# Kernel tuning notes

Measured on AMD Instinct MI355X. Metric: run time of the kernel, lower is better.

Reference implementation:

```python
import jax, jax.numpy as jnp
import numpy as np

HEADS = 12
DIM = 768


def setup_inputs() -> dict:
    key = jax.random.key(0)
    ks = jax.random.split(key, 11)
    B, T, D, H = 2, 2048, DIM, HEADS
    s = 0.02
    inp = {
        "x": jax.random.normal(ks[0], (B, T, D), dtype=jnp.float32),
        "Wq": jax.random.normal(ks[1], (D, D), dtype=jnp.float32) * s,
        "bq": jax.random.normal(ks[2], (D,), dtype=jnp.float32) * s,
        "Wk": jax.random.normal(ks[3], (D, D), dtype=jnp.float32) * s,
        "bk": jax.random.normal(ks[4], (D,), dtype=jnp.float32) * s,
        "Wv": jax.random.normal(ks[5], (D, D), dtype=jnp.float32) * s,
        "bv": jax.random.normal(ks[6], (D,), dtype=jnp.float32) * s,
        # shaped-attention affine params (torch init: alpha=1, beta=0, gamma=0;
        # perturb so all terms are exercised)
        "alpha": jnp.ones((1, H, 1, 1), jnp.float32) + 0.1 * jax.random.normal(ks[7], (1, H, 1, 1)),
        "beta": 0.1 * jax.random.normal(ks[8], (1, H, 1, 1), dtype=jnp.float32),
        "gamma": 0.1 * jax.random.normal(ks[9], (1, H, 1, 1), dtype=jnp.float32),
        # registered buffer C (zeros in the source)
        "C": jnp.zeros((H, 1, 1), jnp.float32),
    }
    return inp


def reference(x, Wq, bq, Wk, bk, Wv, bv, alpha, beta, gamma, C):
    B, T, D = x.shape
    H = HEADS
    hd = D // H
    scale = hd ** -0.5
    # torch nn.Linear: y = x @ W.T + b ; then [B,T,H,hd] -> [B,H,T,hd]
    q = (x @ Wq.T + bq).reshape(B, T, H, hd).transpose(0, 2, 1, 3)
    k = (x @ Wk.T + bk).reshape(B, T, H, hd).transpose(0, 2, 1, 3)
    v = (x @ Wv.T + bv).reshape(B, T, H, hd).transpose(0, 2, 1, 3)
    attn = jax.nn.softmax(jnp.einsum("bhqd,bhkd->bhqk", q, k) * scale, axis=-1)
    # shaped correction: alpha*I + beta*softmax - gamma*C
    eye = jnp.eye(T, dtype=x.dtype)
    attn = alpha * eye + beta * attn - gamma * C  # C:(H,1,1) broadcasts over T,T
    out = jnp.einsum("bhqk,bhkd->bhqd", attn, v)
    return out.transpose(0, 2, 1, 3).reshape(B, T, D)
```

## Files before the change

kernel.cpp:

```cpp
#include <hip/hip_runtime.h>
#include <hip/hip_bf16.h>

#define HEADS 12
#define HD 64
#define DMODEL 768
#define TSEQ 2048
#define BATCH 2
#define NTOK (BATCH*TSEQ)
#define NQKV (3*DMODEL)
#define KSPLIT 4
#define BK 64
#define KVBLK 64

typedef __attribute__((ext_vector_type(8))) short bf16x8;
typedef __attribute__((ext_vector_type(4))) short bf16x4;
typedef __attribute__((ext_vector_type(4))) float f32x4;
typedef __attribute__((ext_vector_type(16))) float f32x16;
typedef __attribute__((ext_vector_type(2))) unsigned uint32x2;

static __device__ inline float bf2f(short s) {
  union { float f; unsigned u; } cv; cv.u = ((unsigned)(unsigned short)s) << 16; return cv.f;
}
static __device__ inline short f2bf(float f) {
  union { float f; unsigned u; } cv; cv.f = f;
  unsigned u = cv.u;
  unsigned r = u + 0x7FFF + ((u >> 16) & 1);
  return (short)(r >> 16);
}

__global__ void cvt_kernel(const float* __restrict__ x,
                           const float* __restrict__ Wq, const float* __restrict__ Wk,
                           const float* __restrict__ Wv,
                           const float* __restrict__ bq, const float* __restrict__ bk,
                           const float* __restrict__ bv,
                           short* __restrict__ Xb, short* __restrict__ Wc,
                           float* __restrict__ bc) {
  const int NX4 = NTOK*DMODEL/4;
  const int WSZ = DMODEL*DMODEL;
  const int NW4 = 3*WSZ/4;
  const int total = NX4 + NW4 + NQKV;
  for (int i = blockIdx.x*blockDim.x + threadIdx.x; i < total; i += gridDim.x*blockDim.x) {
    if (i < NX4) {
      f32x4 v = *(const f32x4*)&x[i*4];
      bf16x4 o;
      #pragma unroll
      for (int j=0;j<4;j++) o[j] = f2bf(v[j]);
      *(bf16x4*)&Xb[i*4] = o;
    } else if (i < NX4 + NW4) {
      int j = (i - NX4)*4;
      const float* src = (j < WSZ) ? &Wq[j] : (j < 2*WSZ) ? &Wk[j - WSZ] : &Wv[j - 2*WSZ];
      f32x4 v = *(const f32x4*)src;
      bf16x4 o;
      #pragma unroll
      for (int jj=0;jj<4;jj++) o[jj] = f2bf(v[jj]);
      *(bf16x4*)&Wc[j] = o;
    } else {
      int o = i - NX4 - NW4;
      bc[o] = (o < DMODEL) ? bq[o] : (o < 2*DMODEL) ? bk[o - DMODEL] : bv[o - 2*DMODEL];
    }
  }
}

__global__ __launch_bounds__(256,2) void qkv_gemm(const short* __restrict__ Xb,
                                                  const short* __restrict__ Wc,
                                                  const float* __restrict__ bc,
                                                  short* __restrict__ Q, short* __restrict__ K,
                                                  short* __restrict__ V, short* __restrict__ Vt) {
  __shared__ __align__(16) char lds[65536];
  const int nbn = NQKV/128;
  int swzb = ((blockIdx.x & 7) * 72) + (blockIdx.x >> 3);
  int bm = swzb / nbn, bn = swzb % nbn;
  int trow = bm*128, tcol = bn*128;
  int tid = threadIdx.x;
  int w = tid >> 6, l = tid & 63;
  int wr = w >> 1, wc = w & 1;
  int lr = l & 15, lg = l >> 4;

  int rbase = tid >> 3;
  int csw   = (tid & 7) ^ (rbase & 7);
  const short* pA = Xb + (size_t)(trow + rbase)*DMODEL + csw*8;
  const short* pB = Wc + (size_t)(tcol + rbase)*DMODEL + csw*8;

  unsigned aoff[4][2], boff[4][2];
  #pragma unroll
  for (int m=0;m<4;m++)
    #pragma unroll
    for (int kc2=0;kc2<2;kc2++) {
      int rowa = wr*64 + m*16 + lr;
      aoff[m][kc2] = rowa*128 + (((kc2*4+lg) ^ (rowa&7))*16);
      int rowb = wc*64 + m*16 + lr;
      boff[m][kc2] = rowb*128 + (((kc2*4+lg) ^ (rowb&7))*16);
    }

  f32x4 acc[4][4];
  #pragma unroll
  for (int m=0;m<4;m++)
    #pragma unroll
    for (int n=0;n<4;n++) acc[m][n] = (f32x4)0.f;

  auto stage = [&](int buf, int ks) {
    int k0 = ks*BK;
    unsigned base = (unsigned)buf*32768u;
    #pragma unroll
    for (int i=0;i<4;i++) {
      __builtin_amdgcn_global_load_lds(
        (const __attribute__((address_space(1))) unsigned int*)(pA + k0 + i*(32*DMODEL)),
        (__attribute__((address_space(3))) unsigned int*)(lds + base + (i*256 + w*64)*16),
        16, 0, 0);
      __builtin_amdgcn_global_load_lds(
        (const __attribute__((address_space(1))) unsigned int*)(pB + k0 + i*(32*DMODEL)),
        (__attribute__((address_space(3))) unsigned int*)(lds + base + 16384 + (i*256 + w*64)*16),
        16, 0, 0);
    }
  };

  stage(0, 0);
  asm volatile("s_waitcnt vmcnt(0)");
  __syncthreads();

  const int NKS = DMODEL/BK;
  for (int ks = 0; ks < NKS; ks++) {
    int cur = ks & 1;
    if (ks + 1 < NKS) stage(cur ^ 1, ks + 1);
    unsigned abase = (unsigned)cur*32768u, bbase = abase + 16384u;
    bf16x8 af[4][2], bfr[4][2];
    #pragma unroll
    for (int m=0;m<4;m++)
      #pragma unroll
      for (int kc2=0;kc2<2;kc2++) {
        af[m][kc2]  = *(const bf16x8*)(lds + abase + aoff[m][kc2]);
        bfr[m][kc2] = *(const bf16x8*)(lds + bbase + boff[m][kc2]);
      }
    __builtin_amdgcn_s_setprio(1);
    #pragma unroll
    for (int m=0;m<4;m++)
      #pragma unroll
      for (int n=0;n<4;n++)
        #pragma unroll
        for (int kc2=0;kc2<2;kc2++)
          acc[m][n] = __builtin_amdgcn_mfma_f32_16x16x32_bf16(af[m][kc2], bfr[n][kc2], acc[m][n], 0, 0, 0);
    __builtin_amdgcn_s_setprio(0);
    __syncthreads();
  }

  short* ltile = (short*)lds;
  float bcv[4];
  #pragma unroll
  for (int n=0;n<4;n++) bcv[n] = bc[tcol + wc*64 + n*16 + lr];
  #pragma unroll
  for (int m=0;m<4;m++)
    #pragma unroll
    for (int n=0;n<4;n++)
      #pragma unroll
      for (int j=0;j<4;j++)
        ltile[(wr*64 + m*16 + lg*4 + j)*128 + wc*64 + n*16 + lr] = f2bf(acc[m][n][j] + bcv[n]);
  __syncthreads();

  int sel = tcol / DMODEL;
  int h0  = (tcol % DMODEL) >> 6;
  short* dstQKV = (sel == 0) ? Q : (sel == 1) ? K : V;
  #pragma unroll
  for (int rr=0; rr<8; rr++) {
    int idx = rr*256 + tid;
    int r2 = idx >> 4, c2 = idx & 15;
    int t = trow + r2;
    int b = t >> 11, tt = t & (TSEQ-1);
    int hh = h0 + (c2 >> 3), d0 = (c2 & 7)*8;
    bf16x8 val = *(const bf16x8*)&ltile[r2*128 + c2*8];
    *(bf16x8*)&dstQKV[((size_t)(b*HEADS + hh)*TSEQ + tt)*HD + d0] = val;
  }
  if (sel == 2) {
    #pragma unroll
    for (int rr=0; rr<8; rr++) {
      int idx = rr*256 + tid;
      int col = idx >> 4, tc8 = idx & 15;
      int hh = h0 + (col >> 6), d = col & 63;
      int t0 = trow + tc8*8;
      int b = t0 >> 11, tt0 = t0 & (TSEQ-1);
      bf16x8 v;
      #pragma unroll
      for (int j=0;j<8;j++) v[j] = ltile[(tc8*8 + j)*128 + col];
      *(bf16x8*)&Vt[((size_t)(b*HEADS + hh)*HD + d)*TSEQ + tt0] = v;
    }
  }
}

__global__ __launch_bounds__(256) void vsum1(const short* __restrict__ V, float* __restrict__ part) {
  int bh = blockIdx.x >> 3, tc = blockIdx.x & 7;
  int d = threadIdx.x & 63, tg = threadIdx.x >> 6;
  const short* p = V + ((size_t)bh*TSEQ + tc*256)*HD + d;
  float s = 0.f;
  #pragma unroll 8
  for (int i = 0; i < 64; i++) s += bf2f(p[(size_t)(tg + i*4)*HD]);
  __shared__ float red[4][64];
  red[tg][d] = s;
  __syncthreads();
  if (tg == 0) part[(bh*8 + tc)*64 + d] = red[0][d] + red[1][d] + red[2][d] + red[3][d];
}
__global__ void vsum2(const float* __restrict__ part, float* __restrict__ vs) {
  int bh = blockIdx.x, d = threadIdx.x;
  float s = 0.f;
  for (int c = 0; c < 8; c++) s += part[(bh*8 + c)*64 + d];
  vs[bh*64 + d] = s;
}

__global__ __launch_bounds__(256,3) void attn_kernel(
    const short* __restrict__ Q, const short* __restrict__ K,
    const short* __restrict__ Vt,
    short* __restrict__ po, float* __restrict__ pml) {
  const int nqt = TSEQ/128;
  int bid = blockIdx.x;
  int ks_id = bid % KSPLIT;
  int r = bid / KSPLIT;
  int qt = r % nqt;
  int bh = r / nqt;

  int tid = threadIdx.x;
  int w = tid >> 6, lane = tid & 63;
  int q5 = lane & 31, hi = lane >> 5;
  int qrow = qt*128 + w*32 + q5;

  __shared__ __align__(16) char kbuf[2][8192];
  __shared__ __align__(16) char vbuf[2][8192];

  const short* Qp  = Q  + (size_t)bh*TSEQ*HD;
  const short* Kp  = K  + (size_t)bh*TSEQ*HD;
  const short* Vtp = Vt + (size_t)bh*HD*TSEQ;

  bf16x8 qf[4];
  #pragma unroll
  for (int c=0;c<4;c++)
    qf[c] = *(const bf16x8*)&Qp[(size_t)qrow*HD + c*16 + hi*8];

  const int ksoff = ks_id*(TSEQ/KSPLIT);

  auto stage = [&](int buf, int kt) {
    int kb = ksoff + kt*KVBLK;
    #pragma unroll
    for (int i=0;i<2;i++) {
      int l0 = i*256 + w*64;
      int l  = l0 + lane;
      int rr = l >> 3, cc = l & 7;
      int sk = cc ^ (rr & 7);
      __builtin_amdgcn_global_load_lds(
        (const __attribute__((address_space(1))) unsigned int*)(Kp + (size_t)(kb + rr)*HD + sk*8),
        (__attribute__((address_space(3))) unsigned int*)(kbuf[buf] + l0*16),
        16, 0, 0);
      __builtin_amdgcn_global_load_lds(
        (const __attribute__((address_space(1))) unsigned int*)(Vtp + (size_t)rr*TSEQ + kb + sk*8),
        (__attribute__((address_space(3))) unsigned int*)(vbuf[buf] + l0*16),
        16, 0, 0);
    }
  };

  f32x16 o0 = (f32x16)0.f, o1 = (f32x16)0.f;
  float psum0 = 0.f, psum1 = 0.f;
  const float c1 = 0.125f * 1.44269504f;
  const float c2 = 8.f * 1.44269504f;
  const int rx = q5 & 7;

  stage(0, 0);
  asm volatile("s_waitcnt vmcnt(0)");
  __syncthreads();

  const int NT = TSEQ/KSPLIT/KVBLK;
  for (int kt = 0; kt < NT; kt++) {
    int cur = kt & 1;
    if (kt + 1 < NT) stage(cur ^ 1, kt + 1);

    #pragma unroll
    for (int t=0;t<2;t++) {
      bf16x8 kf[4];
      #pragma unroll
      for (int c=0;c<4;c++)
        kf[c] = *(const bf16x8*)(kbuf[cur] + (t*32+q5)*128 + (((c*2+hi) ^ rx)*16));

      f32x16 st = (f32x16)0.f;
      __builtin_amdgcn_s_setprio(1);
      #pragma unroll
      for (int c=0;c<4;c++)
        st = __builtin_amdgcn_mfma_f32_32x32x16_bf16(kf[c], qf[c], st, 0, 0, 0);
      __builtin_amdgcn_s_setprio(0);

      bf16x8 vf0[2], vf1[2];
      #pragma unroll
      for (int ks2=0;ks2<2;ks2++) {
        int kc = ((t*4 + ks2*2 + hi) ^ rx)*16;
        vf0[ks2] = *(const bf16x8*)(vbuf[cur] + q5*128 + kc);
        vf1[ks2] = *(const bf16x8*)(vbuf[cur] + (q5+32)*128 + kc);
      }

      #pragma unroll
      for (int i=0;i<16;i+=2) {
        st[i]   = __builtin_amdgcn_exp2f(st[i]*c1   - c2);
        st[i+1] = __builtin_amdgcn_exp2f(st[i+1]*c1 - c2);
        psum0 += st[i];
        psum1 += st[i+1];
      }
      unsigned pw[4][2];
      #pragma unroll
      for (int a=0;a<4;a++)
        #pragma unroll
        for (int p=0;p<2;p++) {
          union { __hip_bfloat162 h; unsigned u; } cvp;
          cvp.h = __float22bfloat162_rn(float2{st[a*4+2*p], st[a*4+2*p+1]});
          pw[a][p] = cvp.u;
        }
      #pragma unroll
      for (int ks2=0;ks2<2;ks2++) {
        uint32x2 s0 = __builtin_amdgcn_permlane32_swap(pw[2*ks2][0],   pw[2*ks2][0],   false, false);
        uint32x2 s1 = __builtin_amdgcn_permlane32_swap(pw[2*ks2][1],   pw[2*ks2][1],   false, false);
        uint32x2 s2 = __builtin_amdgcn_permlane32_swap(pw[2*ks2+1][0], pw[2*ks2+1][0], false, false);
        uint32x2 s3 = __builtin_amdgcn_permlane32_swap(pw[2*ks2+1][1], pw[2*ks2+1][1], false, false);
        union { unsigned u[4]; bf16x8 v; } bw;
        bw.u[0] = s0[0];
        bw.u[1] = s1[0];
        bw.u[2] = s2[1];
        bw.u[3] = s3[1];
        __builtin_amdgcn_s_setprio(1);
        o0 = __builtin_amdgcn_mfma_f32_32x32x16_bf16(vf0[ks2], bw.v, o0, 0, 0, 0);
        o1 = __builtin_amdgcn_mfma_f32_32x32x16_bf16(vf1[ks2], bw.v, o1, 0, 0, 0);
        __builtin_amdgcn_s_setprio(0);
      }
    }

    asm volatile("s_waitcnt vmcnt(0)");
    __syncthreads();
  }

  float psum = psum0 + psum1;
  float ltot = psum + __shfl_xor(psum, 32);
  size_t gq = (size_t)bh*TSEQ + qrow;
  if (!hi) pml[gq*KSPLIT + ks_id] = ltot;

  #pragma unroll
  for (int rg=0; rg<4; rg++) {
    bf16x4 pk0, pk1;
    #pragma unroll
    for (int rj=0;rj<4;rj++) { pk0[rj] = f2bf(o0[rg*4+rj]); pk1[rj] = f2bf(o1[rg*4+rj]); }
    int d0 = rg*8 + hi*4;
    *(bf16x4*)&po[(gq*KSPLIT + ks_id)*HD + d0]      = pk0;
    *(bf16x4*)&po[(gq*KSPLIT + ks_id)*HD + 32 + d0] = pk1;
  }
}

__global__ __launch_bounds__(256) void combine_kernel(
    const short* __restrict__ po, const float* __restrict__ pml,
    const short* __restrict__ V, const float* __restrict__ vs,
    const float* __restrict__ alpha, const float* __restrict__ beta,
    const float* __restrict__ gamma, const float* __restrict__ Cc,
    float* __restrict__ out) {
  size_t gq = (size_t)blockIdx.x*4 + (threadIdx.x >> 6);
  int d = threadIdx.x & 63;
  int bh = (int)(gq >> 11), q = (int)(gq & (TSEQ-1));
  int b = bh / HEADS, h = bh % HEADS;

  float L = 0.f, acc = 0.f;
  #pragma unroll
  for (int i=0;i<KSPLIT;i++) {
    L   += pml[gq*KSPLIT + i];
    acc += bf2f(po[(gq*KSPLIT + i)*HD + d]);
  }
  float sv = acc / L;
  float al = alpha[h], be = beta[h], ga = gamma[h], cc = Cc[h];
  float vv = bf2f(V[((size_t)bh*TSEQ + q)*HD + d]);
  out[((size_t)b*TSEQ + q)*DMODEL + h*HD + d] = al*vv + be*sv - ga*cc*vs[bh*HD + d];
}

extern "C" void kernel_launch(void* const* d_in, const int* in_sizes, int n_in,
                              void* d_out, int out_size, void* d_ws, size_t ws_size,
                              hipStream_t stream) {
  const float* x     = (const float*)d_in[0];
  const float* Wq    = (const float*)d_in[1];
  const float* bq    = (const float*)d_in[2];
  const float* Wk    = (const float*)d_in[3];
  const float* bk    = (const float*)d_in[4];
  const float* Wv    = (const float*)d_in[5];
  const float* bv    = (const float*)d_in[6];
  const float* alpha = (const float*)d_in[7];
  const float* beta  = (const float*)d_in[8];
  const float* gamma = (const float*)d_in[9];
  const float* Cc    = (const float*)d_in[10];
  float* out = (float*)d_out;

  char* ws = (char*)d_ws;
  size_t off = 0;
  auto alloc = [&](size_t bytes) -> void* {
    void* p = ws + off; off += (bytes + 255) & ~(size_t)255; return p;
  };
  short* Xb = (short*)alloc((size_t)NTOK*DMODEL*2);
  short* Wc = (short*)alloc((size_t)NQKV*DMODEL*2);
  float* bc = (float*)alloc((size_t)NQKV*4);
  short* Q  = (short*)alloc((size_t)BATCH*HEADS*TSEQ*HD*2);
  short* K  = (short*)alloc((size_t)BATCH*HEADS*TSEQ*HD*2);
  short* V  = (short*)alloc((size_t)BATCH*HEADS*TSEQ*HD*2);
  short* Vt = (short*)alloc((size_t)BATCH*HEADS*TSEQ*HD*2);
  float* vs = (float*)alloc((size_t)BATCH*HEADS*HD*4);
  float* part = (float*)alloc((size_t)BATCH*HEADS*8*HD*4);
  short* po  = (short*)alloc((size_t)BATCH*HEADS*TSEQ*KSPLIT*HD*2);
  float* pml = (float*)alloc((size_t)BATCH*HEADS*TSEQ*KSPLIT*4);

  cvt_kernel<<<1024, 256, 0, stream>>>(x, Wq, Wk, Wv, bq, bk, bv, Xb, Wc, bc);
  qkv_gemm<<<(NTOK/128)*(NQKV/128), 256, 0, stream>>>(Xb, Wc, bc, Q, K, V, Vt);
  vsum1<<<BATCH*HEADS*8, 256, 0, stream>>>(V, part);
  vsum2<<<BATCH*HEADS, 64, 0, stream>>>(part, vs);
  attn_kernel<<<BATCH*HEADS*(TSEQ/128)*KSPLIT, 256, 0, stream>>>(Q, K, Vt, po, pml);
  combine_kernel<<<BATCH*HEADS*TSEQ/4, 256, 0, stream>>>(po, pml, V, vs, alpha, beta, gamma, Cc, out);
}
```

Baseline: 96.09 us.

## Fuse V column sums into QKV GEMM epilogue and vectorize combine kernel

Drops the two-stage vsum kernels. The column sum of V is now computed from the LDS tile in the QKV GEMM epilogue and accumulated with atomicAdd into a buffer that is zeroed by a memset. The combine kernel now has each thread handle 8 output elements using bf16x8 and f32x4 vector loads and stores, giving 8x fewer blocks. This removes two kernel launches and one re-read of V, at the cost of atomics and the float summation order no longer being deterministic.

```diff
diff --git a/kernel.cpp b/kernel.cpp
--- a/kernel.cpp
+++ b/kernel.cpp
@@ -65,7 +65,8 @@
                                                   const short* __restrict__ Wc,
                                                   const float* __restrict__ bc,
                                                   short* __restrict__ Q, short* __restrict__ K,
-                                                  short* __restrict__ V, short* __restrict__ Vt) {
+                                                  short* __restrict__ V, short* __restrict__ Vt,
+                                                  float* __restrict__ vs) {
   __shared__ __align__(16) char lds[65536];
   const int nbn = NQKV/128;
   int swzb = ((blockIdx.x & 7) * 72) + (blockIdx.x >> 3);
@@ -182,26 +183,15 @@
       for (int j=0;j<8;j++) v[j] = ltile[(tc8*8 + j)*128 + col];
       *(bf16x8*)&Vt[((size_t)(b*HEADS + hh)*HD + d)*TSEQ + tt0] = v;
     }
-  }
-}
-
-__global__ __launch_bounds__(256) void vsum1(const short* __restrict__ V, float* __restrict__ part) {
-  int bh = blockIdx.x >> 3, tc = blockIdx.x & 7;
-  int d = threadIdx.x & 63, tg = threadIdx.x >> 6;
-  const short* p = V + ((size_t)bh*TSEQ + tc*256)*HD + d;
-  float s = 0.f;
-  #pragma unroll 8
-  for (int i = 0; i < 64; i++) s += bf2f(p[(size_t)(tg + i*4)*HD]);
-  __shared__ float red[4][64];
-  red[tg][d] = s;
-  __syncthreads();
-  if (tg == 0) part[(bh*8 + tc)*64 + d] = red[0][d] + red[1][d] + red[2][d] + red[3][d];
-}
-__global__ void vsum2(const float* __restrict__ part, float* __restrict__ vs) {
-  int bh = blockIdx.x, d = threadIdx.x;
-  float s = 0.f;
-  for (int c = 0; c < 8; c++) s += part[(bh*8 + c)*64 + d];
-  vs[bh*64 + d] = s;
+    int col = tid & 127;
+    int rh  = tid >> 7;
+    float s = 0.f;
+    #pragma unroll
+    for (int i=0;i<64;i++) s += bf2f(ltile[(rh*64 + i)*128 + col]);
+    int hh = h0 + (col >> 6), d = col & 63;
+    int b = trow >> 11;
+    atomicAdd(&vs[(b*HEADS + hh)*HD + d], s);
+  }
 }
 
 __global__ __launch_bounds__(256,3) void attn_kernel(
@@ -350,21 +340,35 @@
     const float* __restrict__ alpha, const float* __restrict__ beta,
     const float* __restrict__ gamma, const float* __restrict__ Cc,
     float* __restrict__ out) {
-  size_t gq = (size_t)blockIdx.x*4 + (threadIdx.x >> 6);
-  int d = threadIdx.x & 63;
+  int t = threadIdx.x;
+  size_t gq = (size_t)blockIdx.x*32 + (t >> 3);
+  int d0 = (t & 7)*8;
   int bh = (int)(gq >> 11), q = (int)(gq & (TSEQ-1));
   int b = bh / HEADS, h = bh % HEADS;
 
-  float L = 0.f, acc = 0.f;
+  float L = 0.f;
+  float acc[8] = {0,0,0,0,0,0,0,0};
   #pragma unroll
   for (int i=0;i<KSPLIT;i++) {
-    L   += pml[gq*KSPLIT + i];
-    acc += bf2f(po[(gq*KSPLIT + i)*HD + d]);
-  }
-  float sv = acc / L;
-  float al = alpha[h], be = beta[h], ga = gamma[h], cc = Cc[h];
-  float vv = bf2f(V[((size_t)bh*TSEQ + q)*HD + d]);
-  out[((size_t)b*TSEQ + q)*DMODEL + h*HD + d] = al*vv + be*sv - ga*cc*vs[bh*HD + d];
+    L += pml[gq*KSPLIT + i];
+    bf16x8 p8 = *(const bf16x8*)&po[(gq*KSPLIT + i)*HD + d0];
+    #pragma unroll
+    for (int j=0;j<8;j++) acc[j] += bf2f(p8[j]);
+  }
+  float inv = 1.f / L;
+  float al = alpha[h], be = beta[h], gc = gamma[h]*Cc[h];
+  bf16x8 v8 = *(const bf16x8*)&V[((size_t)bh*TSEQ + q)*HD + d0];
+  f32x4 vs0 = *(const f32x4*)&vs[bh*HD + d0];
+  f32x4 vs1 = *(const f32x4*)&vs[bh*HD + d0 + 4];
+  f32x4 r0, r1;
+  #pragma unroll
+  for (int j=0;j<4;j++) {
+    r0[j] = al*bf2f(v8[j])   + be*acc[j]*inv   - gc*vs0[j];
+    r1[j] = al*bf2f(v8[j+4]) + be*acc[j+4]*inv - gc*vs1[j];
+  }
+  float* op = &out[((size_t)b*TSEQ + q)*DMODEL + h*HD + d0];
+  *(f32x4*)op = r0;
+  *(f32x4*)(op+4) = r1;
 }
 
 extern "C" void kernel_launch(void* const* d_in, const int* in_sizes, int n_in,
@@ -396,14 +400,12 @@
   short* V  = (short*)alloc((size_t)BATCH*HEADS*TSEQ*HD*2);
   short* Vt = (short*)alloc((size_t)BATCH*HEADS*TSEQ*HD*2);
   float* vs = (float*)alloc((size_t)BATCH*HEADS*HD*4);
-  float* part = (float*)alloc((size_t)BATCH*HEADS*8*HD*4);
   short* po  = (short*)alloc((size_t)BATCH*HEADS*TSEQ*KSPLIT*HD*2);
   float* pml = (float*)alloc((size_t)BATCH*HEADS*TSEQ*KSPLIT*4);
 
+  hipMemsetAsync(vs, 0, (size_t)BATCH*HEADS*HD*4, stream);
   cvt_kernel<<<1024, 256, 0, stream>>>(x, Wq, Wk, Wv, bq, bk, bv, Xb, Wc, bc);
-  qkv_gemm<<<(NTOK/128)*(NQKV/128), 256, 0, stream>>>(Xb, Wc, bc, Q, K, V, Vt);
-  vsum1<<<BATCH*HEADS*8, 256, 0, stream>>>(V, part);
-  vsum2<<<BATCH*HEADS, 64, 0, stream>>>(part, vs);
+  qkv_gemm<<<(NTOK/128)*(NQKV/128), 256, 0, stream>>>(Xb, Wc, bc, Q, K, V, Vt, vs);
   attn_kernel<<<BATCH*HEADS*(TSEQ/128)*KSPLIT, 256, 0, stream>>>(Q, K, Vt, po, pml);
-  combine_kernel<<<BATCH*HEADS*TSEQ/4, 256, 0, stream>>>(po, pml, V, vs, alpha, beta, gamma, Cc, out);
-}
+  combine_kernel<<<BATCH*HEADS*TSEQ/32, 256, 0, stream>>>(po, pml, V, vs, alpha, beta, gamma, Cc, out);
+}
```

Result: faster. 94.09 us (-2.1%).
